# Kernel tuning notes

Measured on AMD Instinct MI355X. Metric: run time of the kernel, lower is better.

The kernel has to match this reference:

```python
import jax, jax.numpy as jnp
import numpy as np

CUBE_SIZE = 24
N_NEURONS = CUBE_SIZE ** 3  # 13824
INPUT_DIM = 512
OUTPUT_DIM = 1000
MAX_STEPS = 30
BATCH = 256


def _build_neighbor_indices(size: int) -> np.ndarray:
    """[N, 27] int32; invalid (out-of-cube) neighbors map to pad slot N."""
    n = size ** 3
    c = np.arange(size)
    z, y, x = np.meshgrid(c, c, c, indexing='ij')  # each [size,size,size]
    cols = []
    for dz in (-1, 0, 1):
        for dy in (-1, 0, 1):
            for dx in (-1, 0, 1):
                nz, ny, nx = z + dz, y + dy, x + dx
                valid = ((nz >= 0) & (nz < size) & (ny >= 0) & (ny < size)
                         & (nx >= 0) & (nx < size))
                idx = nz * size * size + ny * size + nx
                cols.append(np.where(valid, idx, n))
    return np.stack(cols, axis=-1).reshape(n, 27).astype(np.int32)


def setup_inputs() -> dict:
    key = jax.random.key(0)
    ks = jax.random.split(key, 4)
    # xavier-ish small init scales (gain 0.5 style)
    w_in = jax.random.normal(ks[0], (N_NEURONS, INPUT_DIM), jnp.float32) * 0.01
    w_local = jax.random.normal(ks[1], (N_NEURONS, 27), jnp.float32) * 0.1
    w_out = jax.random.normal(ks[2], (OUTPUT_DIM, N_NEURONS), jnp.float32) * 0.01
    x = jax.random.normal(ks[3], (BATCH, INPUT_DIM), jnp.float32)
    return {
        'x': x,
        'W_in_w': w_in,
        'W_in_b': jnp.zeros((N_NEURONS,), jnp.float32),
        'W_local': w_local,
        'W_out_w': w_out,
        'W_out_b': jnp.zeros((OUTPUT_DIM,), jnp.float32),
        'neighbor_indices': jnp.asarray(_build_neighbor_indices(CUBE_SIZE)),
    }


def reference(x, W_in_w, W_in_b, W_local, W_out_w, W_out_b, neighbor_indices):
    batch = x.shape[0]
    x_proj = x @ W_in_w.T + W_in_b  # [B, N]
    h0 = jnp.zeros((batch, N_NEURONS), x.dtype)
    pad = jnp.zeros((batch, 1), x.dtype)

    def step(h, _):
        h_padded = jnp.concatenate([h, pad], axis=1)        # [B, N+1]
        nbr = h_padded[:, neighbor_indices]                  # [B, N, 27]
        weighted = jnp.einsum('bnk,nk->bn', nbr, W_local)    # [B, N]
        return jnp.tanh(x_proj + weighted), None

    h, _ = jax.lax.scan(step, h0, None, length=MAX_STEPS)
    return h @ W_out_w.T + W_out_b  # [B, output_dim]
```

## Files before the change

### kernel.cpp

```cpp
#include <hip/hip_runtime.h>
#include <hip/hip_bf16.h>

#define NN   13824
#define BB   256
#define KDIM 512
#define ODIM 1000
#define CUBE 24
#define KS   16
#define XSTR 520
#define OSTR 456

typedef short bf8 __attribute__((ext_vector_type(8)));
typedef float f32x4 __attribute__((ext_vector_type(4)));

__device__ __forceinline__ float fast_tanh(float a) {
    float e = __expf(2.0f * a);
    return 1.0f - 2.0f / (e + 1.0f);
}
__device__ __forceinline__ float bf_lo(unsigned u) { return __uint_as_float(u << 16); }
__device__ __forceinline__ float bf_hi(unsigned u) { return __uint_as_float(u & 0xffff0000u); }
__device__ __forceinline__ unsigned short bf_rne(float f) {
    unsigned u = __float_as_uint(f);
    u += 0x7fffu + ((u >> 16) & 1u);
    return (unsigned short)(u >> 16);
}
__device__ __forceinline__ unsigned pk_bf16(float lo, float hi) {
    union { __hip_bfloat162 h; unsigned u; } cv;
    cv.h = __float22bfloat162_rn(make_float2(lo, hi));
    return cv.u;
}

__global__ __launch_bounds__(256) void xbf_kernel(
    const float* __restrict__ x, unsigned* __restrict__ xb)
{
    int i = blockIdx.x * 256 + threadIdx.x;
    float2 v = *(const float2*)&x[(size_t)i * 2];
    xb[i] = pk_bf16(v.x, v.y);
}

__global__ __launch_bounds__(256) void xproj_mfma(
    const float* __restrict__ w_in, const float* __restrict__ bias,
    const short* __restrict__ xbf, unsigned short* __restrict__ xp,
    unsigned short* __restrict__ h1)
{
    __shared__ unsigned short As[16 * XSTR];
    const int tid = threadIdx.x, w = tid >> 6, lane = tid & 63;
    const int quad = lane >> 4, l16 = lane & 15;
    const int n0 = blockIdx.x * 16;

#pragma unroll
    for (int rr = 0; rr < 4; ++rr) {
        const int row = w * 4 + rr;
        const float* __restrict__ src = &w_in[(size_t)(n0 + row) * KDIM];
#pragma unroll
        for (int c = 0; c < 2; ++c) {
            const int col = c * 256 + lane * 4;
            float4 v = *(const float4*)&src[col];
            uint2 pk2 = make_uint2(pk_bf16(v.x, v.y), pk_bf16(v.z, v.w));
            *(uint2*)&As[row * XSTR + col] = pk2;
        }
    }
    __syncthreads();

    f32x4 acc[4] = {};

    int ka = quad * 8;
    bf8 bb[4];
#pragma unroll
    for (int j = 0; j < 4; ++j)
        bb[j] = *(const bf8*)&xbf[(size_t)(w * 64 + j * 16 + l16) * KDIM + ka];

    for (int it = 0; it < 16; ++it) {
        bf8 nb[4] = {};
        if (it < 15) {
            const int nka = ka + 32;
#pragma unroll
            for (int j = 0; j < 4; ++j)
                nb[j] = *(const bf8*)&xbf[(size_t)(w * 64 + j * 16 + l16) * KDIM + nka];
        }
        bf8 af = *(const bf8*)&As[l16 * XSTR + it * 32 + quad * 8];
#pragma unroll
        for (int j = 0; j < 4; ++j)
            acc[j] = __builtin_amdgcn_mfma_f32_16x16x32_bf16(af, bb[j], acc[j], 0, 0, 0);
#pragma unroll
        for (int j = 0; j < 4; ++j) bb[j] = nb[j];
        ka += 32;
    }

#pragma unroll
    for (int j = 0; j < 4; ++j) {
        const int b = w * 64 + j * 16 + l16;
#pragma unroll
        for (int r = 0; r < 4; ++r) {
            const int n = n0 + quad * 4 + r;
            const float v = acc[j][r] + bias[n];
            xp[(size_t)n * BB + b] = bf_rne(v);
            h1[(size_t)n * BB + b] = bf_rne(fast_tanh(v));
        }
    }
}

__device__ __forceinline__ void load_plane_f2(
    const unsigned* __restrict__ h32, int z, int y, int xx, int dof, float2* w9)
{
#pragma unroll
    for (int j = 0; j < 9; ++j) {
        const int dz = j / 3 - 1, dy = j % 3 - 1;
        const int zz = z + dz, yy = y + dy;
        const bool valid = (xx >= 0) & (xx < CUBE) & (zz >= 0) & (zz < CUBE) &
                           (yy >= 0) & (yy < CUBE);
        unsigned v = 0u;
        if (valid) v = h32[(size_t)((zz * 24 + yy) * 24 + xx) * 128 + dof];
        w9[j] = make_float2(bf_lo(v), bf_hi(v));
    }
}

__global__ __launch_bounds__(256) void step_kernel(
    const unsigned* __restrict__ hprev, const unsigned* __restrict__ xp,
    const float* __restrict__ wl, unsigned* __restrict__ hnext)
{
    const int tid  = threadIdx.x;
    const int wid  = __builtin_amdgcn_readfirstlane(tid >> 6);
    const int wvb  = wid & 1;
    const int yoff = wid >> 1;
    const int lane = tid & 63;

    const int bid   = blockIdx.x;
    const int zhi   = bid & 7;
    const int inner = bid >> 3;
    const int yp    = inner % 12;
    const int r     = inner / 12;
    const int xc    = r & 3;
    const int zlo   = r >> 2;
    const int z     = zhi * 3 + zlo;
    const int y     = yp * 2 + yoff;

    const int x0   = xc * 6;
    const int dof  = wvb * 64 + lane;

    float2 win[5][9];
    load_plane_f2(hprev, z, y, x0 - 1, dof, win[0]);
    load_plane_f2(hprev, z, y, x0,     dof, win[1]);
    load_plane_f2(hprev, z, y, x0 + 1, dof, win[2]);
    load_plane_f2(hprev, z, y, x0 + 2, dof, win[3]);

#pragma unroll
    for (int xi = 0; xi < 6; ++xi) {
        const int x = x0 + xi;
        if (xi <= 3)
            load_plane_f2(hprev, z, y, x + 3, dof, win[(xi + 4) % 5]);

        const int n = (z * 24 + y) * 24 + x;
        const float* __restrict__ wn = &wl[(size_t)n * 27];
        const unsigned xpv = xp[(size_t)n * 128 + dof];
        float2 acc = make_float2(bf_lo(xpv), bf_hi(xpv));

        const float2* pm = win[xi % 5];
        const float2* pc = win[(xi + 1) % 5];
        const float2* pp = win[(xi + 2) % 5];
#pragma unroll
        for (int j = 0; j < 9; ++j) {
            const float w0 = wn[3 * j + 0];
            const float w1 = wn[3 * j + 1];
            const float w2 = wn[3 * j + 2];
            acc.x += w0 * pm[j].x + w1 * pc[j].x + w2 * pp[j].x;
            acc.y += w0 * pm[j].y + w1 * pc[j].y + w2 * pp[j].y;
        }
        hnext[(size_t)n * 128 + dof] = pk_bf16(fast_tanh(acc.x), fast_tanh(acc.y));
    }
}

__global__ __launch_bounds__(256) void transpose_kernel(
    const unsigned* __restrict__ h32, unsigned* __restrict__ hT32)
{
    __shared__ unsigned short T[64][66];
    const int tid = threadIdx.x;
    const int rr = tid >> 2, g = tid & 3;
    const int k0 = blockIdx.x * 64, b0 = blockIdx.y * 64;
#pragma unroll
    for (int i = 0; i < 8; ++i) {
        unsigned d = h32[(size_t)(k0 + rr) * 128 + b0 / 2 + g * 8 + i];
        const int bl = (g * 8 + i) * 2;
        T[bl][rr]     = (unsigned short)(d & 0xffffu);
        T[bl + 1][rr] = (unsigned short)(d >> 16);
    }
    __syncthreads();
#pragma unroll
    for (int i = 0; i < 8; ++i) {
        const int kl = (g * 8 + i) * 2;
        unsigned d = (unsigned)T[rr][kl] | ((unsigned)T[rr][kl + 1] << 16);
        hT32[(size_t)(b0 + rr) * (NN / 2) + k0 / 2 + g * 8 + i] = d;
    }
}

__global__ __launch_bounds__(512) void outgemm_mfma(
    const float* __restrict__ wout, const short* __restrict__ hT,
    float* __restrict__ part)
{
    __shared__ unsigned short As[128 * OSTR];
    const int tid = threadIdx.x, w = tid >> 6, lane = tid & 63;
    const int quad = lane >> 4, l16 = lane & 15;
    const int kb = blockIdx.x * (NN / KS);
    const int o0 = blockIdx.y * 128;
    const int b0 = w * 32;

    f32x4 acc[8][2] = {};

#pragma unroll 1
    for (int ph = 0; ph < 2; ++ph) {
        const int poff  = ph ? 448 : 0;
        const int pcols = ph ? 416 : 448;
        const int pkc   = ph ? 13 : 14;
        if (ph) __syncthreads();

#pragma unroll 4
        for (int rr = 0; rr < 16; ++rr) {
            const int row = w * 16 + rr;
            const int o = o0 + row;
            const float* __restrict__ src = &wout[(size_t)o * NN + kb + poff];
            {
                const int col = lane * 4;
                float4 v = {0.f, 0.f, 0.f, 0.f};
                if (o < ODIM) v = *(const float4*)&src[col];
                *(uint2*)&As[row * OSTR + col] =
                    make_uint2(pk_bf16(v.x, v.y), pk_bf16(v.z, v.w));
            }
            {
                const int col = 256 + lane * 4;
                if (col < pcols) {
                    float4 v = {0.f, 0.f, 0.f, 0.f};
                    if (o < ODIM) v = *(const float4*)&src[col];
                    *(uint2*)&As[row * OSTR + col] =
                        make_uint2(pk_bf16(v.x, v.y), pk_bf16(v.z, v.w));
                }
            }
        }
        __syncthreads();

        bf8 b0f, b1f;
        {
            const int ka = kb + poff + quad * 8;
            b0f = *(const bf8*)&hT[(size_t)(b0 + l16) * NN + ka];
            b1f = *(const bf8*)&hT[(size_t)(b0 + 16 + l16) * NN + ka];
        }
        for (int kc = 0; kc < pkc; ++kc) {
            bf8 n0 = {}, n1 = {};
            if (kc + 1 < pkc) {
                const int ka = kb + poff + (kc + 1) * 32 + quad * 8;
                n0 = *(const bf8*)&hT[(size_t)(b0 + l16) * NN + ka];
                n1 = *(const bf8*)&hT[(size_t)(b0 + 16 + l16) * NN + ka];
            }
            const int cs = kc * 32 + quad * 8;
#pragma unroll
            for (int t = 0; t < 8; ++t) {
                bf8 af = *(const bf8*)&As[(t * 16 + l16) * OSTR + cs];
                acc[t][0] = __builtin_amdgcn_mfma_f32_16x16x32_bf16(af, b0f, acc[t][0], 0, 0, 0);
                acc[t][1] = __builtin_amdgcn_mfma_f32_16x16x32_bf16(af, b1f, acc[t][1], 0, 0, 0);
            }
            b0f = n0; b1f = n1;
        }
    }

#pragma unroll
    for (int t = 0; t < 8; ++t)
#pragma unroll
        for (int j = 0; j < 2; ++j) {
            const int b = b0 + j * 16 + l16;
#pragma unroll
            for (int r = 0; r < 4; ++r) {
                const int o = o0 + t * 16 + quad * 4 + r;
                part[((size_t)blockIdx.x * 1024 + o) * BB + b] = acc[t][j][r];
            }
        }
}

__global__ __launch_bounds__(256) void reduce_kernel(
    const float* __restrict__ part, const float* __restrict__ bias,
    float* __restrict__ out)
{
    const int o = blockIdx.x, b = threadIdx.x;
    float s = bias[o];
#pragma unroll
    for (int kc = 0; kc < KS; ++kc)
        s += part[((size_t)kc * 1024 + o) * BB + b];
    out[(size_t)b * ODIM + o] = s;
}

extern "C" void kernel_launch(void* const* d_in, const int* in_sizes, int n_in,
                              void* d_out, int out_size, void* d_ws, size_t ws_size,
                              hipStream_t stream)
{
    const float* x       = (const float*)d_in[0];
    const float* w_in    = (const float*)d_in[1];
    const float* b_in    = (const float*)d_in[2];
    const float* w_local = (const float*)d_in[3];
    const float* w_out   = (const float*)d_in[4];
    const float* b_out   = (const float*)d_in[5];
    float* out = (float*)d_out;

    char* p = (char*)d_ws;
    unsigned short* xp_bf = (unsigned short*)p;          p += (size_t)NN * BB * 2;
    unsigned short* hA    = (unsigned short*)p;          p += (size_t)NN * BB * 2;
    unsigned short* hB    = (unsigned short*)p;          p += (size_t)NN * BB * 2;
    unsigned short* hT    = (unsigned short*)p;          p += (size_t)NN * BB * 2;
    unsigned short* x_bf  = (unsigned short*)p;          p += (size_t)BB * KDIM * 2;
    float*          part  = (float*)p;

    xbf_kernel<<<256, 256, 0, stream>>>(x, (unsigned*)x_bf);
    xproj_mfma<<<864, 256, 0, stream>>>(w_in, b_in, (const short*)x_bf, xp_bf, hA);

    const unsigned* hp = (const unsigned*)hA;
    unsigned* hn = (unsigned*)hB;
    for (int s = 0; s < 29; ++s) {
        step_kernel<<<1152, 256, 0, stream>>>(hp, (const unsigned*)xp_bf, w_local, hn);
        unsigned* t = (unsigned*)hp; hp = hn; hn = t;
    }

    transpose_kernel<<<dim3(216, 4), 256, 0, stream>>>(hp, (unsigned*)hT);
    outgemm_mfma<<<dim3(KS, 8), 512, 0, stream>>>(w_out, (const short*)hT, part);
    reduce_kernel<<<ODIM, 256, 0, stream>>>(part, b_out, out);
}
```

Before: 553.8 us.

## Split output GEMM over batch halves and adjust LDS strides

The output GEMM grid gains a z dimension of two batch halves, so each wave handles 16 batch columns instead of 32. This doubles the block count from 128 to 256 for better CU coverage, at the cost of each block re-converting its W_out tile to bf16 twice overall. The shared-memory row strides XSTR and OSTR are also changed, likely to alter bank-conflict patterns.

```diff
diff --git a/kernel.cpp b/kernel.cpp
--- a/kernel.cpp
+++ b/kernel.cpp
@@ -7,8 +7,8 @@
 #define ODIM 1000
 #define CUBE 24
 #define KS   16
-#define XSTR 520
-#define OSTR 456
+#define XSTR 516
+#define OSTR 452
 
 typedef short bf8 __attribute__((ext_vector_type(8)));
 typedef float f32x4 __attribute__((ext_vector_type(4)));
@@ -202,9 +202,9 @@
     const int quad = lane >> 4, l16 = lane & 15;
     const int kb = blockIdx.x * (NN / KS);
     const int o0 = blockIdx.y * 128;
-    const int b0 = w * 32;
-
-    f32x4 acc[8][2] = {};
+    const int b0 = blockIdx.z * 128 + w * 16;
+
+    f32x4 acc[8] = {};
 
 #pragma unroll 1
     for (int ph = 0; ph < 2; ++ph) {
@@ -218,15 +218,9 @@
             const int row = w * 16 + rr;
             const int o = o0 + row;
             const float* __restrict__ src = &wout[(size_t)o * NN + kb + poff];
-            {
-                const int col = lane * 4;
-                float4 v = {0.f, 0.f, 0.f, 0.f};
-                if (o < ODIM) v = *(const float4*)&src[col];
-                *(uint2*)&As[row * OSTR + col] =
-                    make_uint2(pk_bf16(v.x, v.y), pk_bf16(v.z, v.w));
-            }
-            {
-                const int col = 256 + lane * 4;
+#pragma unroll
+            for (int c = 0; c < 2; ++c) {
+                const int col = c * 256 + lane * 4;
                 if (col < pcols) {
                     float4 v = {0.f, 0.f, 0.f, 0.f};
                     if (o < ODIM) v = *(const float4*)&src[col];
@@ -237,41 +231,36 @@
         }
         __syncthreads();
 
-        bf8 b0f, b1f;
+        bf8 bb;
         {
             const int ka = kb + poff + quad * 8;
-            b0f = *(const bf8*)&hT[(size_t)(b0 + l16) * NN + ka];
-            b1f = *(const bf8*)&hT[(size_t)(b0 + 16 + l16) * NN + ka];
+            bb = *(const bf8*)&hT[(size_t)(b0 + l16) * NN + ka];
         }
         for (int kc = 0; kc < pkc; ++kc) {
-            bf8 n0 = {}, n1 = {};
+            bf8 nb = {};
             if (kc + 1 < pkc) {
                 const int ka = kb + poff + (kc + 1) * 32 + quad * 8;
-                n0 = *(const bf8*)&hT[(size_t)(b0 + l16) * NN + ka];
-                n1 = *(const bf8*)&hT[(size_t)(b0 + 16 + l16) * NN + ka];
+                nb = *(const bf8*)&hT[(size_t)(b0 + l16) * NN + ka];
             }
             const int cs = kc * 32 + quad * 8;
 #pragma unroll
             for (int t = 0; t < 8; ++t) {
                 bf8 af = *(const bf8*)&As[(t * 16 + l16) * OSTR + cs];
-                acc[t][0] = __builtin_amdgcn_mfma_f32_16x16x32_bf16(af, b0f, acc[t][0], 0, 0, 0);
-                acc[t][1] = __builtin_amdgcn_mfma_f32_16x16x32_bf16(af, b1f, acc[t][1], 0, 0, 0);
+                acc[t] = __builtin_amdgcn_mfma_f32_16x16x32_bf16(af, bb, acc[t], 0, 0, 0);
             }
-            b0f = n0; b1f = n1;
-        }
-    }
-
-#pragma unroll
-    for (int t = 0; t < 8; ++t)
-#pragma unroll
-        for (int j = 0; j < 2; ++j) {
-            const int b = b0 + j * 16 + l16;
-#pragma unroll
-            for (int r = 0; r < 4; ++r) {
-                const int o = o0 + t * 16 + quad * 4 + r;
-                part[((size_t)blockIdx.x * 1024 + o) * BB + b] = acc[t][j][r];
-            }
-        }
+            bb = nb;
+        }
+    }
+
+#pragma unroll
+    for (int t = 0; t < 8; ++t) {
+        const int b = b0 + l16;
+#pragma unroll
+        for (int r = 0; r < 4; ++r) {
+            const int o = o0 + t * 16 + quad * 4 + r;
+            part[((size_t)blockIdx.x * 1024 + o) * BB + b] = acc[t][r];
+        }
+    }
 }
 
 __global__ __launch_bounds__(256) void reduce_kernel(
@@ -317,6 +306,6 @@
     }
 
     transpose_kernel<<<dim3(216, 4), 256, 0, stream>>>(hp, (unsigned*)hT);
-    outgemm_mfma<<<dim3(KS, 8), 512, 0, stream>>>(w_out, (const short*)hT, part);
+    outgemm_mfma<<<dim3(KS, 8, 2), 512, 0, stream>>>(w_out, (const short*)hT, part);
     reduce_kernel<<<ODIM, 256, 0, stream>>>(part, b_out, out);
 }
```

Result: no change. 547.3 us (-1.2%).
